# Kernel optimization log

Measured on AMD Instinct MI355X. Metric: run time of the kernel, lower is better.

Reference implementation:

```python
import jax, jax.numpy as jnp
import numpy as np

T, H, E, K, I = 4096, 1024, 8, 2, 2048
EPS = 1e-5


def setup_inputs() -> dict:
    key = jax.random.key(0)
    ks = jax.random.split(key, 5)
    xavier = jax.nn.initializers.variance_scaling(1.0, 'fan_avg', 'uniform', dtype=jnp.float32)
    return {
        'x': jax.random.normal(ks[0], (T, H), dtype=jnp.float32),
        'scale': jnp.ones((H,), dtype=jnp.float32),
        'gate_kernel': xavier(ks[1], (H, E), jnp.float32),
        'gate_bias': jnp.zeros((E,), dtype=jnp.float32),
        'mlp1_weight': xavier(ks[2], (E, 2 * I, H), jnp.float32),
        'mlp1_bias': jnp.zeros((E, 2 * I), dtype=jnp.float32),
        'mlp2_weight': xavier(ks[3], (E, H, I), jnp.float32),
        'mlp2_bias': jnp.zeros((E, H), dtype=jnp.float32),
    }


def reference(x, scale, gate_kernel, gate_bias, mlp1_weight, mlp1_bias, mlp2_weight, mlp2_bias):
    # RMSNorm in fp32
    t = x.astype(jnp.float32)
    rms = jnp.sqrt(jnp.mean(t * t, axis=-1, keepdims=True) + EPS)
    normed = ((t / rms) * scale).astype(x.dtype)  # [T, H]

    # Gating: top-k experts + softmax over selected logits
    gate_logits = normed @ gate_kernel + gate_bias  # [T, E]
    expert_logits, expert_indices = jax.lax.top_k(gate_logits, K)  # [T, K]
    expert_weights = jax.nn.softmax(expert_logits, axis=-1)  # [T, K]

    # Dense all-expert SwiGLU MLP (faithful to vmap-over-experts original)
    # mlp1_weight: [E, 2I, H] -> mlp1: [E, T, 2I]
    mlp1 = jnp.einsum('td,efd->etf', normed, mlp1_weight) + mlp1_bias[:, None, :]
    gate_part = jnp.minimum(mlp1[..., :I], 7.0)
    linear_part = jnp.clip(mlp1[..., I:], -7.0, 7.0)
    swish_gate = gate_part * jax.nn.sigmoid(1.702 * gate_part)
    activated = swish_gate * (linear_part + 1.0)  # [E, T, I]
    # mlp2_weight: [E, H, I] -> expert_outputs: [T, E, H]
    expert_outputs = (jnp.einsum('eti,ehi->eth', activated, mlp2_weight)
                      + mlp2_bias[:, None, :]).transpose(1, 0, 2)

    # Scatter top-k weights to dense [T, E] and combine
    one_hot = jax.nn.one_hot(expert_indices, E, dtype=expert_outputs.dtype)  # [T, K, E]
    dense_gate_weights = jnp.sum(one_hot * expert_weights[..., None], axis=1)  # [T, E]
    fused = jnp.einsum('teh,te->th', expert_outputs, dense_gate_weights)
    return x + fused
```

## Files before the change

### kernel.cpp

```cpp
#include <hip/hip_runtime.h>
#include <hip/hip_bf16.h>
#include <math.h>

#define T_ 4096
#define H_ 1024
#define E_ 8
#define I_ 2048
#define EPS_ 1e-5f

using bf16x8 = __attribute__((ext_vector_type(8))) short;
using f32x4  = __attribute__((ext_vector_type(4))) float;

static __device__ __forceinline__ unsigned short f2bf(float f) {
    union { float f; unsigned int u; } v; v.f = f;
    unsigned int u = v.u;
    u += 0x7fffu + ((u >> 16) & 1u);
    return (unsigned short)(u >> 16);
}

__global__ __launch_bounds__(256) void k_convert(
    const float* __restrict__ src, unsigned short* __restrict__ dst)
{
    size_t i = (size_t)blockIdx.x * 256 + threadIdx.x;
    const float4* s = (const float4*)src + i * 2;
    float4 a = s[0], b = s[1];
    ushort4 lo, hi;
    lo.x = f2bf(a.x); lo.y = f2bf(a.y); lo.z = f2bf(a.z); lo.w = f2bf(a.w);
    hi.x = f2bf(b.x); hi.y = f2bf(b.y); hi.z = f2bf(b.z); hi.w = f2bf(b.w);
    ((ushort4*)dst)[i * 2]     = lo;
    ((ushort4*)dst)[i * 2 + 1] = hi;
}

__global__ __launch_bounds__(256) void k_norm_gate(
    const float* __restrict__ x, const float* __restrict__ scale,
    const float* __restrict__ gk, const float* __restrict__ gb,
    unsigned short* __restrict__ normed_bf,
    int* __restrict__ counts, int* __restrict__ tok_list, float* __restrict__ wtok)
{
    int tid = threadIdx.x;
    int wave = tid >> 6, lane = tid & 63;
    int t = blockIdx.x * 4 + wave;
    const float* xr = x + (size_t)t * H_;
    int h0 = lane * 16;

    float4 xv[4], sv[4];
    #pragma unroll
    for (int c = 0; c < 4; c++) {
        xv[c] = *(const float4*)(xr + h0 + c * 4);
        sv[c] = *(const float4*)(scale + h0 + c * 4);
    }
    float ss = 0.f;
    #pragma unroll
    for (int c = 0; c < 4; c++)
        ss += xv[c].x*xv[c].x + xv[c].y*xv[c].y + xv[c].z*xv[c].z + xv[c].w*xv[c].w;
    #pragma unroll
    for (int off = 32; off; off >>= 1) ss += __shfl_xor(ss, off);
    float inv = 1.0f / sqrtf(ss / (float)H_ + EPS_);

    float nv[16];
    #pragma unroll
    for (int c = 0; c < 4; c++) {
        nv[c*4+0] = xv[c].x * inv * sv[c].x;
        nv[c*4+1] = xv[c].y * inv * sv[c].y;
        nv[c*4+2] = xv[c].z * inv * sv[c].z;
        nv[c*4+3] = xv[c].w * inv * sv[c].w;
    }
    #pragma unroll
    for (int c = 0; c < 4; c++) {
        ushort4 nb;
        nb.x = f2bf(nv[c*4+0]); nb.y = f2bf(nv[c*4+1]);
        nb.z = f2bf(nv[c*4+2]); nb.w = f2bf(nv[c*4+3]);
        *(ushort4*)(normed_bf + (size_t)t * H_ + h0 + c * 4) = nb;
    }

    float p[E_];
    #pragma unroll
    for (int e = 0; e < E_; e++) p[e] = 0.f;
    #pragma unroll
    for (int j = 0; j < 16; j++) {
        const float4* g4 = (const float4*)(gk + (size_t)(h0 + j) * E_);
        float4 a = g4[0], b = g4[1];
        float n = nv[j];
        p[0] += n*a.x; p[1] += n*a.y; p[2] += n*a.z; p[3] += n*a.w;
        p[4] += n*b.x; p[5] += n*b.y; p[6] += n*b.z; p[7] += n*b.w;
    }
    #pragma unroll
    for (int e = 0; e < E_; e++) {
        #pragma unroll
        for (int off = 32; off; off >>= 1) p[e] += __shfl_xor(p[e], off);
    }
    if (lane == 0) {
        int b0 = -1, b1 = -1; float l0 = -1e30f, l1 = -1e30f;
        #pragma unroll
        for (int e = 0; e < E_; e++) {
            float lg = p[e] + gb[e];
            if (lg > l0) { l1 = l0; b1 = b0; l0 = lg; b0 = e; }
            else if (lg > l1) { l1 = lg; b1 = e; }
        }
        float e1 = expf(l1 - l0);
        float w0 = 1.f / (1.f + e1);
        float w1 = e1 / (1.f + e1);
        wtok[t * 2 + 0] = w0;
        wtok[t * 2 + 1] = w1;
        int p0 = atomicAdd(&counts[b0], 1);
        tok_list[b0 * T_ + p0] = t * 2 + 0;
        int p1 = atomicAdd(&counts[b1], 1);
        tok_list[b1 * T_ + p1] = t * 2 + 1;
    }
}

__global__ __launch_bounds__(256) void k_mlp1(
    const unsigned short* __restrict__ w1b,
    const float* __restrict__ b1,
    const unsigned short* __restrict__ normed_bf,
    const int* __restrict__ counts, const int* __restrict__ tok_list,
    unsigned short* __restrict__ act)
{
    int e = blockIdx.z;
    int Ne = counts[e];
    int mt0 = blockIdx.y * 64;
    if (mt0 >= Ne) return;
    int it0 = blockIdx.x * 64;
    int tid = threadIdx.x;
    int lane = tid & 63, w = tid >> 6;
    int quad = lane >> 4, m16 = lane & 15;
    int wr = w >> 1, wc = w & 1;

    __shared__ unsigned short lA[64 * 64];
    __shared__ unsigned short lBg[64 * 64];
    __shared__ unsigned short lBl[64 * 64];
    __shared__ int ls_tk[64];

    if (tid < 64) {
        int slot = mt0 + tid;
        ls_tk[tid] = (slot < Ne) ? tok_list[e * T_ + slot] : -1;
    }
    __syncthreads();

    f32x4 accg[2][2], accl[2][2];
    #pragma unroll
    for (int mi = 0; mi < 2; mi++)
        #pragma unroll
        for (int ni = 0; ni < 2; ni++) {
            accg[mi][ni] = (f32x4){0.f, 0.f, 0.f, 0.f};
            accl[mi][ni] = (f32x4){0.f, 0.f, 0.f, 0.f};
        }

    const size_t w1base = (size_t)e * 2 * I_ * H_;
    int rA = tid >> 3, sgA = tid & 7;
    int nB = tid >> 2, sgB = tid & 3;
    int jA = sgA ^ (rA & 7);
    int jB0 = (2 * sgB) ^ (nB & 7);
    int jB1 = (2 * sgB + 1) ^ (nB & 7);

    int tk0 = ls_tk[rA], tk1 = ls_tk[rA + 32];
    const unsigned short* sA0 = normed_bf + (size_t)((tk0 < 0) ? 0 : (tk0 >> 1)) * H_ + sgA * 8;
    const unsigned short* sA1 = normed_bf + (size_t)((tk1 < 0) ? 0 : (tk1 >> 1)) * H_ + sgA * 8;
    const unsigned short* sG = w1b + w1base + (size_t)(it0 + nB) * H_ + sgB * 16;
    const unsigned short* sL = sG + (size_t)I_ * H_;

    uint4 ra0, ra1, rg0, rg1, rl0, rl1;
    ra0 = (tk0 >= 0) ? *(const uint4*)(sA0) : make_uint4(0,0,0,0);
    ra1 = (tk1 >= 0) ? *(const uint4*)(sA1) : make_uint4(0,0,0,0);
    rg0 = ((const uint4*)sG)[0]; rg1 = ((const uint4*)sG)[1];
    rl0 = ((const uint4*)sL)[0]; rl1 = ((const uint4*)sL)[1];

    for (int kk = 0; kk < H_; kk += 64) {
        __syncthreads();
        *(uint4*)(&lA[rA * 64 + jA * 8])          = ra0;
        *(uint4*)(&lA[(rA + 32) * 64 + jA * 8])   = ra1;
        *(uint4*)(&lBg[nB * 64 + jB0 * 8])        = rg0;
        *(uint4*)(&lBg[nB * 64 + jB1 * 8])        = rg1;
        *(uint4*)(&lBl[nB * 64 + jB0 * 8])        = rl0;
        *(uint4*)(&lBl[nB * 64 + jB1 * 8])        = rl1;
        __syncthreads();
        if (kk + 64 < H_) {
            int k2 = kk + 64;
            ra0 = (tk0 >= 0) ? *(const uint4*)(sA0 + k2) : make_uint4(0,0,0,0);
            ra1 = (tk1 >= 0) ? *(const uint4*)(sA1 + k2) : make_uint4(0,0,0,0);
            rg0 = ((const uint4*)(sG + k2))[0]; rg1 = ((const uint4*)(sG + k2))[1];
            rl0 = ((const uint4*)(sL + k2))[0]; rl1 = ((const uint4*)(sL + k2))[1];
        }
        #pragma unroll
        for (int ks2 = 0; ks2 < 2; ks2++) {
            int jj = ks2 * 4 + quad;
            int m7 = m16 & 7;
            bf16x8 af[2], bg[2], bl[2];
            #pragma unroll
            for (int mi = 0; mi < 2; mi++)
                af[mi] = *(const bf16x8*)(&lA[(wr * 32 + mi * 16 + m16) * 64 + (jj ^ m7) * 8]);
            #pragma unroll
            for (int ni = 0; ni < 2; ni++) {
                bg[ni] = *(const bf16x8*)(&lBg[(wc * 32 + ni * 16 + m16) * 64 + (jj ^ m7) * 8]);
                bl[ni] = *(const bf16x8*)(&lBl[(wc * 32 + ni * 16 + m16) * 64 + (jj ^ m7) * 8]);
            }
            #pragma unroll
            for (int mi = 0; mi < 2; mi++)
                #pragma unroll
                for (int ni = 0; ni < 2; ni++) {
                    accg[mi][ni] = __builtin_amdgcn_mfma_f32_16x16x32_bf16(
                        af[mi], bg[ni], accg[mi][ni], 0, 0, 0);
                    accl[mi][ni] = __builtin_amdgcn_mfma_f32_16x16x32_bf16(
                        af[mi], bl[ni], accl[mi][ni], 0, 0, 0);
                }
        }
    }

    const float* b1g = b1 + (size_t)e * 2 * I_;
    const float* b1l = b1g + I_;
    #pragma unroll
    for (int mi = 0; mi < 2; mi++) {
        #pragma unroll
        for (int reg = 0; reg < 4; reg++) {
            int row = wr * 32 + mi * 16 + quad * 4 + reg;
            int tk = ls_tk[row];
            if (tk < 0) continue;
            #pragma unroll
            for (int ni = 0; ni < 2; ni++) {
                int i = it0 + wc * 32 + ni * 16 + m16;
                float g = accg[mi][ni][reg] + b1g[i];
                float l = accl[mi][ni][reg] + b1l[i];
                g = fminf(g, 7.f);
                l = fminf(fmaxf(l, -7.f), 7.f);
                float sw = g / (1.f + expf(-1.702f * g));
                act[(size_t)tk * I_ + i] = f2bf(sw * (l + 1.f));
            }
        }
    }
}

__global__ __launch_bounds__(256) void k_mlp2(
    const unsigned short* __restrict__ w2b,
    const float* __restrict__ b2,
    const unsigned short* __restrict__ act,
    const int* __restrict__ counts, const int* __restrict__ tok_list,
    float* __restrict__ ybuf)
{
    int e = blockIdx.z;
    int Ne = counts[e];
    int mt0 = blockIdx.y * 64;
    if (mt0 >= Ne) return;
    int ht0 = blockIdx.x * 128;
    int tid = threadIdx.x;
    int lane = tid & 63, w = tid >> 6;
    int quad = lane >> 4, m16 = lane & 15;
    int wr = w >> 1, wc = w & 1;

    __shared__ unsigned short lA[64 * 64];
    __shared__ unsigned short lB[128 * 64];
    __shared__ int ls_tk[64];

    if (tid < 64) {
        int slot = mt0 + tid;
        ls_tk[tid] = (slot < Ne) ? tok_list[e * T_ + slot] : -1;
    }
    __syncthreads();

    f32x4 acc[2][4];
    #pragma unroll
    for (int mi = 0; mi < 2; mi++)
        #pragma unroll
        for (int ni = 0; ni < 4; ni++)
            acc[mi][ni] = (f32x4){0.f, 0.f, 0.f, 0.f};

    const size_t w2base = (size_t)e * H_ * I_;
    int rA = tid >> 3, sgA = tid & 7;
    int nB = tid >> 2, sgB = tid & 3;
    int jA = sgA ^ (rA & 7);
    int jB0 = (2 * sgB) ^ (nB & 7);
    int jB1 = (2 * sgB + 1) ^ (nB & 7);

    int tk0 = ls_tk[rA], tk1 = ls_tk[rA + 32];
    const unsigned short* sA0 = act + (size_t)((tk0 < 0) ? 0 : tk0) * I_ + sgA * 8;
    const unsigned short* sA1 = act + (size_t)((tk1 < 0) ? 0 : tk1) * I_ + sgA * 8;
    const unsigned short* sB0 = w2b + w2base + (size_t)(ht0 + nB) * I_ + sgB * 16;
    const unsigned short* sB1 = sB0 + (size_t)64 * I_;

    uint4 ra0, ra1, rb00, rb01, rb10, rb11;
    ra0 = (tk0 >= 0) ? *(const uint4*)(sA0) : make_uint4(0,0,0,0);
    ra1 = (tk1 >= 0) ? *(const uint4*)(sA1) : make_uint4(0,0,0,0);
    rb00 = ((const uint4*)sB0)[0]; rb01 = ((const uint4*)sB0)[1];
    rb10 = ((const uint4*)sB1)[0]; rb11 = ((const uint4*)sB1)[1];

    for (int kk = 0; kk < I_; kk += 64) {
        __syncthreads();
        *(uint4*)(&lA[rA * 64 + jA * 8])               = ra0;
        *(uint4*)(&lA[(rA + 32) * 64 + jA * 8])        = ra1;
        *(uint4*)(&lB[nB * 64 + jB0 * 8])              = rb00;
        *(uint4*)(&lB[nB * 64 + jB1 * 8])              = rb01;
        *(uint4*)(&lB[(nB + 64) * 64 + jB0 * 8])       = rb10;
        *(uint4*)(&lB[(nB + 64) * 64 + jB1 * 8])       = rb11;
        __syncthreads();
        if (kk + 64 < I_) {
            int k2 = kk + 64;
            ra0 = (tk0 >= 0) ? *(const uint4*)(sA0 + k2) : make_uint4(0,0,0,0);
            ra1 = (tk1 >= 0) ? *(const uint4*)(sA1 + k2) : make_uint4(0,0,0,0);
            rb00 = ((const uint4*)(sB0 + k2))[0]; rb01 = ((const uint4*)(sB0 + k2))[1];
            rb10 = ((const uint4*)(sB1 + k2))[0]; rb11 = ((const uint4*)(sB1 + k2))[1];
        }
        #pragma unroll
        for (int ks2 = 0; ks2 < 2; ks2++) {
            int jj = ks2 * 4 + quad;
            int m7 = m16 & 7;
            bf16x8 af[2], bf[4];
            #pragma unroll
            for (int mi = 0; mi < 2; mi++)
                af[mi] = *(const bf16x8*)(&lA[(wr * 32 + mi * 16 + m16) * 64 + (jj ^ m7) * 8]);
            #pragma unroll
            for (int ni = 0; ni < 4; ni++)
                bf[ni] = *(const bf16x8*)(&lB[(wc * 64 + ni * 16 + m16) * 64 + (jj ^ m7) * 8]);
            #pragma unroll
            for (int mi = 0; mi < 2; mi++)
                #pragma unroll
                for (int ni = 0; ni < 4; ni++)
                    acc[mi][ni] = __builtin_amdgcn_mfma_f32_16x16x32_bf16(
                        af[mi], bf[ni], acc[mi][ni], 0, 0, 0);
        }
    }

    const float* b2e = b2 + (size_t)e * H_;
    #pragma unroll
    for (int mi = 0; mi < 2; mi++) {
        #pragma unroll
        for (int reg = 0; reg < 4; reg++) {
            int row = wr * 32 + mi * 16 + quad * 4 + reg;
            int tk = ls_tk[row];
            if (tk < 0) continue;
            #pragma unroll
            for (int ni = 0; ni < 4; ni++) {
                int h = ht0 + wc * 64 + ni * 16 + m16;
                ybuf[(size_t)tk * H_ + h] = acc[mi][ni][reg] + b2e[h];
            }
        }
    }
}

__global__ __launch_bounds__(256) void k_combine(
    const float* __restrict__ x, const float* __restrict__ ybuf,
    const float* __restrict__ wtok, float* __restrict__ out)
{
    int t = blockIdx.x;
    int tid = threadIdx.x;
    float w0 = wtok[t * 2 + 0];
    float w1 = wtok[t * 2 + 1];
    float4 xv = ((const float4*)(x + (size_t)t * H_))[tid];
    float4 y0 = ((const float4*)(ybuf + (size_t)(t * 2) * H_))[tid];
    float4 y1 = ((const float4*)(ybuf + (size_t)(t * 2 + 1) * H_))[tid];
    float4 o;
    o.x = xv.x + w0 * y0.x + w1 * y1.x;
    o.y = xv.y + w0 * y0.y + w1 * y1.y;
    o.z = xv.z + w0 * y0.z + w1 * y1.z;
    o.w = xv.w + w0 * y0.w + w1 * y1.w;
    ((float4*)(out + (size_t)t * H_))[tid] = o;
}

extern "C" void kernel_launch(void* const* d_in, const int* in_sizes, int n_in,
                              void* d_out, int out_size, void* d_ws, size_t ws_size,
                              hipStream_t stream) {
    const float* x     = (const float*)d_in[0];
    const float* scale = (const float*)d_in[1];
    const float* gk    = (const float*)d_in[2];
    const float* gb    = (const float*)d_in[3];
    const float* w1    = (const float*)d_in[4];
    const float* b1    = (const float*)d_in[5];
    const float* w2    = (const float*)d_in[6];
    const float* b2    = (const float*)d_in[7];
    float* out = (float*)d_out;

    char* ws = (char*)d_ws;
    const size_t MB = 1024 * 1024;
    unsigned short* normed_bf = (unsigned short*)ws;
    unsigned short* act       = (unsigned short*)(ws + 8 * MB);
    unsigned short* w1b       = (unsigned short*)(ws + 40 * MB);
    float*          ybuf      = (float*)(ws + 40 * MB);
    unsigned short* w2b       = (unsigned short*)(ws + 104 * MB);
    char* ctl                 = ws + 136 * MB;
    int*   counts   = (int*)ctl;
    int*   tok_list = (int*)(ctl + 256);
    float* wtok     = (float*)(ctl + 256 + (size_t)E_ * T_ * 4);

    hipMemsetAsync(counts, 0, E_ * sizeof(int), stream);

    k_norm_gate<<<dim3(T_ / 4), dim3(256), 0, stream>>>(
        x, scale, gk, gb, normed_bf, counts, tok_list, wtok);
    k_convert<<<dim3((E_ * 2 * I_ * H_) / (256 * 8)), dim3(256), 0, stream>>>(w1, w1b);
    k_convert<<<dim3((E_ * H_ * I_) / (256 * 8)), dim3(256), 0, stream>>>(w2, w2b);

    k_mlp1<<<dim3(I_ / 64, T_ / 64, E_), dim3(256), 0, stream>>>(
        w1b, b1, normed_bf, counts, tok_list, act);
    k_mlp2<<<dim3(H_ / 128, T_ / 64, E_), dim3(256), 0, stream>>>(
        w2b, b2, act, counts, tok_list, ybuf);
    k_combine<<<dim3(T_), dim3(256), 0, stream>>>(x, ybuf, wtok, out);
}
```

Measured before the change: 567.9 us.

## Use direct global-to-LDS loads and double token tile in MoE GEMMs

```diff
diff --git a/kernel.cpp b/kernel.cpp
--- a/kernel.cpp
+++ b/kernel.cpp
@@ -16,6 +16,13 @@
     unsigned int u = v.u;
     u += 0x7fffu + ((u >> 16) & 1u);
     return (unsigned short)(u >> 16);
+}
+
+static __device__ __forceinline__ void gld16(const unsigned short* g, unsigned short* l) {
+    __builtin_amdgcn_global_load_lds(
+        (const __attribute__((address_space(1))) unsigned int*)g,
+        (__attribute__((address_space(3))) unsigned int*)l,
+        16, 0, 0);
 }
 
 __global__ __launch_bounds__(256) void k_convert(
@@ -118,7 +125,7 @@
 {
     int e = blockIdx.z;
     int Ne = counts[e];
-    int mt0 = blockIdx.y * 64;
+    int mt0 = blockIdx.y * 128;
     if (mt0 >= Ne) return;
     int it0 = blockIdx.x * 64;
     int tid = threadIdx.x;
@@ -126,76 +133,72 @@
     int quad = lane >> 4, m16 = lane & 15;
     int wr = w >> 1, wc = w & 1;
 
-    __shared__ unsigned short lA[64 * 64];
+    __shared__ unsigned short lA[128 * 64];
     __shared__ unsigned short lBg[64 * 64];
     __shared__ unsigned short lBl[64 * 64];
-    __shared__ int ls_tk[64];
-
-    if (tid < 64) {
+    __shared__ int ls_tk[128];
+
+    if (tid < 128) {
         int slot = mt0 + tid;
         ls_tk[tid] = (slot < Ne) ? tok_list[e * T_ + slot] : -1;
     }
-    __syncthreads();
-
-    f32x4 accg[2][2], accl[2][2];
-    #pragma unroll
-    for (int mi = 0; mi < 2; mi++)
+
+    int lr = lane >> 3;
+    int pc = lane & 7;
+
+    const unsigned short* srcA[4];
+    #pragma unroll
+    for (int it = 0; it < 4; it++) {
+        int r = w * 32 + it * 8 + lr;
+        int slot = mt0 + r;
+        int tk = (slot < Ne) ? tok_list[e * T_ + slot] : 0;
+        srcA[it] = normed_bf + (size_t)(tk >> 1) * H_ + ((pc ^ (r & 7)) << 3);
+    }
+    const size_t w1base = (size_t)e * 2 * I_ * H_;
+    const unsigned short* srcG[2];
+    const unsigned short* srcL[2];
+    #pragma unroll
+    for (int it = 0; it < 2; it++) {
+        int r = w * 16 + it * 8 + lr;
+        srcG[it] = w1b + w1base + (size_t)(it0 + r) * H_ + ((pc ^ (r & 7)) << 3);
+        srcL[it] = srcG[it] + (size_t)I_ * H_;
+    }
+
+    f32x4 accg[4][2], accl[4][2];
+    #pragma unroll
+    for (int mi = 0; mi < 4; mi++)
         #pragma unroll
         for (int ni = 0; ni < 2; ni++) {
             accg[mi][ni] = (f32x4){0.f, 0.f, 0.f, 0.f};
             accl[mi][ni] = (f32x4){0.f, 0.f, 0.f, 0.f};
         }
 
-    const size_t w1base = (size_t)e * 2 * I_ * H_;
-    int rA = tid >> 3, sgA = tid & 7;
-    int nB = tid >> 2, sgB = tid & 3;
-    int jA = sgA ^ (rA & 7);
-    int jB0 = (2 * sgB) ^ (nB & 7);
-    int jB1 = (2 * sgB + 1) ^ (nB & 7);
-
-    int tk0 = ls_tk[rA], tk1 = ls_tk[rA + 32];
-    const unsigned short* sA0 = normed_bf + (size_t)((tk0 < 0) ? 0 : (tk0 >> 1)) * H_ + sgA * 8;
-    const unsigned short* sA1 = normed_bf + (size_t)((tk1 < 0) ? 0 : (tk1 >> 1)) * H_ + sgA * 8;
-    const unsigned short* sG = w1b + w1base + (size_t)(it0 + nB) * H_ + sgB * 16;
-    const unsigned short* sL = sG + (size_t)I_ * H_;
-
-    uint4 ra0, ra1, rg0, rg1, rl0, rl1;
-    ra0 = (tk0 >= 0) ? *(const uint4*)(sA0) : make_uint4(0,0,0,0);
-    ra1 = (tk1 >= 0) ? *(const uint4*)(sA1) : make_uint4(0,0,0,0);
-    rg0 = ((const uint4*)sG)[0]; rg1 = ((const uint4*)sG)[1];
-    rl0 = ((const uint4*)sL)[0]; rl1 = ((const uint4*)sL)[1];
-
     for (int kk = 0; kk < H_; kk += 64) {
         __syncthreads();
-        *(uint4*)(&lA[rA * 64 + jA * 8])          = ra0;
-        *(uint4*)(&lA[(rA + 32) * 64 + jA * 8])   = ra1;
-        *(uint4*)(&lBg[nB * 64 + jB0 * 8])        = rg0;
-        *(uint4*)(&lBg[nB * 64 + jB1 * 8])        = rg1;
-        *(uint4*)(&lBl[nB * 64 + jB0 * 8])        = rl0;
-        *(uint4*)(&lBl[nB * 64 + jB1 * 8])        = rl1;
+        #pragma unroll
+        for (int it = 0; it < 4; it++)
+            gld16(srcA[it] + kk, &lA[(w * 32 + it * 8) * 64]);
+        #pragma unroll
+        for (int it = 0; it < 2; it++) {
+            gld16(srcG[it] + kk, &lBg[(w * 16 + it * 8) * 64]);
+            gld16(srcL[it] + kk, &lBl[(w * 16 + it * 8) * 64]);
+        }
         __syncthreads();
-        if (kk + 64 < H_) {
-            int k2 = kk + 64;
-            ra0 = (tk0 >= 0) ? *(const uint4*)(sA0 + k2) : make_uint4(0,0,0,0);
-            ra1 = (tk1 >= 0) ? *(const uint4*)(sA1 + k2) : make_uint4(0,0,0,0);
-            rg0 = ((const uint4*)(sG + k2))[0]; rg1 = ((const uint4*)(sG + k2))[1];
-            rl0 = ((const uint4*)(sL + k2))[0]; rl1 = ((const uint4*)(sL + k2))[1];
-        }
-        #pragma unroll
-        for (int ks2 = 0; ks2 < 2; ks2++) {
-            int jj = ks2 * 4 + quad;
-            int m7 = m16 & 7;
-            bf16x8 af[2], bg[2], bl[2];
-            #pragma unroll
-            for (int mi = 0; mi < 2; mi++)
-                af[mi] = *(const bf16x8*)(&lA[(wr * 32 + mi * 16 + m16) * 64 + (jj ^ m7) * 8]);
+        int m7 = m16 & 7;
+        #pragma unroll
+        for (int ks = 0; ks < 2; ks++) {
+            int jj = ks * 4 + quad;
+            bf16x8 af[4], bg[2], bl[2];
+            #pragma unroll
+            for (int mi = 0; mi < 4; mi++)
+                af[mi] = *(const bf16x8*)(&lA[(wr * 64 + mi * 16 + m16) * 64 + ((jj ^ m7) << 3)]);
             #pragma unroll
             for (int ni = 0; ni < 2; ni++) {
-                bg[ni] = *(const bf16x8*)(&lBg[(wc * 32 + ni * 16 + m16) * 64 + (jj ^ m7) * 8]);
-                bl[ni] = *(const bf16x8*)(&lBl[(wc * 32 + ni * 16 + m16) * 64 + (jj ^ m7) * 8]);
+                bg[ni] = *(const bf16x8*)(&lBg[(wc * 32 + ni * 16 + m16) * 64 + ((jj ^ m7) << 3)]);
+                bl[ni] = *(const bf16x8*)(&lBl[(wc * 32 + ni * 16 + m16) * 64 + ((jj ^ m7) << 3)]);
             }
             #pragma unroll
-            for (int mi = 0; mi < 2; mi++)
+            for (int mi = 0; mi < 4; mi++)
                 #pragma unroll
                 for (int ni = 0; ni < 2; ni++) {
                     accg[mi][ni] = __builtin_amdgcn_mfma_f32_16x16x32_bf16(
@@ -209,10 +212,10 @@
     const float* b1g = b1 + (size_t)e * 2 * I_;
     const float* b1l = b1g + I_;
     #pragma unroll
-    for (int mi = 0; mi < 2; mi++) {
+    for (int mi = 0; mi < 4; mi++) {
         #pragma unroll
         for (int reg = 0; reg < 4; reg++) {
-            int row = wr * 32 + mi * 16 + quad * 4 + reg;
+            int row = wr * 64 + mi * 16 + quad * 4 + reg;
             int tk = ls_tk[row];
             if (tk < 0) continue;
             #pragma unroll
@@ -238,7 +241,7 @@
 {
     int e = blockIdx.z;
     int Ne = counts[e];
-    int mt0 = blockIdx.y * 64;
+    int mt0 = blockIdx.y * 128;
     if (mt0 >= Ne) return;
     int ht0 = blockIdx.x * 128;
     int tid = threadIdx.x;
@@ -246,84 +249,76 @@
     int quad = lane >> 4, m16 = lane & 15;
     int wr = w >> 1, wc = w & 1;
 
-    __shared__ unsigned short lA[64 * 64];
+    __shared__ unsigned short lA[128 * 64];
     __shared__ unsigned short lB[128 * 64];
-    __shared__ int ls_tk[64];
-
-    if (tid < 64) {
+    __shared__ int ls_tk[128];
+
+    if (tid < 128) {
         int slot = mt0 + tid;
         ls_tk[tid] = (slot < Ne) ? tok_list[e * T_ + slot] : -1;
     }
-    __syncthreads();
-
-    f32x4 acc[2][4];
-    #pragma unroll
-    for (int mi = 0; mi < 2; mi++)
+
+    int lr = lane >> 3;
+    int pc = lane & 7;
+
+    const unsigned short* srcA[4];
+    #pragma unroll
+    for (int it = 0; it < 4; it++) {
+        int r = w * 32 + it * 8 + lr;
+        int slot = mt0 + r;
+        int tk = (slot < Ne) ? tok_list[e * T_ + slot] : 0;
+        srcA[it] = act + (size_t)tk * I_ + ((pc ^ (r & 7)) << 3);
+    }
+    const size_t w2base = (size_t)e * H_ * I_;
+    const unsigned short* srcB[4];
+    #pragma unroll
+    for (int it = 0; it < 4; it++) {
+        int r = w * 32 + it * 8 + lr;
+        srcB[it] = w2b + w2base + (size_t)(ht0 + r) * I_ + ((pc ^ (r & 7)) << 3);
+    }
+
+    f32x4 acc[4][4];
+    #pragma unroll
+    for (int mi = 0; mi < 4; mi++)
         #pragma unroll
         for (int ni = 0; ni < 4; ni++)
             acc[mi][ni] = (f32x4){0.f, 0.f, 0.f, 0.f};
 
-    const size_t w2base = (size_t)e * H_ * I_;
-    int rA = tid >> 3, sgA = tid & 7;
-    int nB = tid >> 2, sgB = tid & 3;
-    int jA = sgA ^ (rA & 7);
-    int jB0 = (2 * sgB) ^ (nB & 7);
-    int jB1 = (2 * sgB + 1) ^ (nB & 7);
-
-    int tk0 = ls_tk[rA], tk1 = ls_tk[rA + 32];
-    const unsigned short* sA0 = act + (size_t)((tk0 < 0) ? 0 : tk0) * I_ + sgA * 8;
-    const unsigned short* sA1 = act + (size_t)((tk1 < 0) ? 0 : tk1) * I_ + sgA * 8;
-    const unsigned short* sB0 = w2b + w2base + (size_t)(ht0 + nB) * I_ + sgB * 16;
-    const unsigned short* sB1 = sB0 + (size_t)64 * I_;
-
-    uint4 ra0, ra1, rb00, rb01, rb10, rb11;
-    ra0 = (tk0 >= 0) ? *(const uint4*)(sA0) : make_uint4(0,0,0,0);
-    ra1 = (tk1 >= 0) ? *(const uint4*)(sA1) : make_uint4(0,0,0,0);
-    rb00 = ((const uint4*)sB0)[0]; rb01 = ((const uint4*)sB0)[1];
-    rb10 = ((const uint4*)sB1)[0]; rb11 = ((const uint4*)sB1)[1];
-
     for (int kk = 0; kk < I_; kk += 64) {
         __syncthreads();
-        *(uint4*)(&lA[rA * 64 + jA * 8])               = ra0;
-        *(uint4*)(&lA[(rA + 32) * 64 + jA * 8])        = ra1;
-        *(uint4*)(&lB[nB * 64 + jB0 * 8])              = rb00;
-        *(uint4*)(&lB[nB * 64 + jB1 * 8])              = rb01;
-        *(uint4*)(&lB[(nB + 64) * 64 + jB0 * 8])       = rb10;
-        *(uint4*)(&lB[(nB + 64) * 64 + jB1 * 8])       = rb11;
+        #pragma unroll
+        for (int it = 0; it < 4; it++)
+            gld16(srcA[it] + kk, &lA[(w * 32 + it * 8) * 64]);
+        #pragma unroll
+        for (int it = 0; it < 4; it++)
+            gld16(srcB[it] + kk, &lB[(w * 32 + it * 8) * 64]);
         __syncthreads();
-        if (kk + 64 < I_) {
-            int k2 = kk + 64;
-            ra0 = (tk0 >= 0) ? *(const uint4*)(sA0 + k2) : make_uint4(0,0,0,0);
-            ra1 = (tk1 >= 0) ? *(const uint4*)(sA1 + k2) : make_uint4(0,0,0,0);
-            rb00 = ((const uint4*)(sB0 + k2))[0]; rb01 = ((const uint4*)(sB0 + k2))[1];
-            rb10 = ((const uint4*)(sB1 + k2))[0]; rb11 = ((const uint4*)(sB1 + k2))[1];
-        }
-        #pragma unroll
-        for (int ks2 = 0; ks2 < 2; ks2++) {
-            int jj = ks2 * 4 + quad;
-            int m7 = m16 & 7;
-            bf16x8 af[2], bf[4];
-            #pragma unroll
-            for (int mi = 0; mi < 2; mi++)
-                af[mi] = *(const bf16x8*)(&lA[(wr * 32 + mi * 16 + m16) * 64 + (jj ^ m7) * 8]);
+        int m7 = m16 & 7;
+        #pragma unroll
+        for (int ks = 0; ks < 2; ks++) {
+            int jj = ks * 4 + quad;
+            bf16x8 af[4], bv[4];
+            #pragma unroll
+            for (int mi = 0; mi < 4; mi++)
+                af[mi] = *(const bf16x8*)(&lA[(wr * 64 + mi * 16 + m16) * 64 + ((jj ^ m7) << 3)]);
             #pragma unroll
             for (int ni = 0; ni < 4; ni++)
-                bf[ni] = *(const bf16x8*)(&lB[(wc * 64 + ni * 16 + m16) * 64 + (jj ^ m7) * 8]);
-            #pragma unroll
-            for (int mi = 0; mi < 2; mi++)
+                bv[ni] = *(const bf16x8*)(&lB[(wc * 64 + ni * 16 + m16) * 64 + ((jj ^ m7) << 3)]);
+            #pragma unroll
+            for (int mi = 0; mi < 4; mi++)
                 #pragma unroll
                 for (int ni = 0; ni < 4; ni++)
                     acc[mi][ni] = __builtin_amdgcn_mfma_f32_16x16x32_bf16(
-                        af[mi], bf[ni], acc[mi][ni], 0, 0, 0);
+                        af[mi], bv[ni], acc[mi][ni], 0, 0, 0);
         }
     }
 
     const float* b2e = b2 + (size_t)e * H_;
     #pragma unroll
-    for (int mi = 0; mi < 2; mi++) {
+    for (int mi = 0; mi < 4; mi++) {
         #pragma unroll
         for (int reg = 0; reg < 4; reg++) {
-            int row = wr * 32 + mi * 16 + quad * 4 + reg;
+            int row = wr * 64 + mi * 16 + quad * 4 + reg;
             int tk = ls_tk[row];
             if (tk < 0) continue;
             #pragma unroll
@@ -386,9 +381,9 @@
     k_convert<<<dim3((E_ * 2 * I_ * H_) / (256 * 8)), dim3(256), 0, stream>>>(w1, w1b);
     k_convert<<<dim3((E_ * H_ * I_) / (256 * 8)), dim3(256), 0, stream>>>(w2, w2b);
 
-    k_mlp1<<<dim3(I_ / 64, T_ / 64, E_), dim3(256), 0, stream>>>(
+    k_mlp1<<<dim3(I_ / 64, T_ / 128, E_), dim3(256), 0, stream>>>(
         w1b, b1, normed_bf, counts, tok_list, act);
-    k_mlp2<<<dim3(H_ / 128, T_ / 64, E_), dim3(256), 0, stream>>>(
+    k_mlp2<<<dim3(H_ / 128, T_ / 128, E_), dim3(256), 0, stream>>>(
         w2b, b2, act, counts, tok_list, ybuf);
     k_combine<<<dim3(T_), dim3(256), 0, stream>>>(x, ybuf, wtok, out);
 }
```

Result: slower. 589.8 us (+3.8%).
